# Kernel optimization log

Measured on AMD Instinct MI355X. Metric: run time of the kernel, lower is better.

## Reference

```python
import jax, jax.numpy as jnp
import numpy as np
from jax import lax


def setup_inputs() -> dict:
    key = jax.random.key(0)
    k1, k2, k3 = jax.random.split(key, 3)
    B, T, dimIn, dimH = 64, 2048, 128, 256
    x = jax.random.normal(k1, (B, T, dimIn), dtype=jnp.float32)
    h = jnp.zeros((B, dimH), dtype=jnp.float32)
    # torch nn.Linear(dimIn+dimH, dimH): weight [dimH, dimIn+dimH], bias [dimH]
    fan_in = dimIn + dimH
    bound = 1.0 / np.sqrt(fan_in)
    W = jax.random.uniform(k2, (dimH, fan_in), minval=-bound, maxval=bound, dtype=jnp.float32)
    b = jax.random.uniform(k3, (dimH,), minval=-bound, maxval=bound, dtype=jnp.float32)
    return {"x": x, "h": h, "W": W, "b": b}


def reference(x, h, W, b):
    # x: [B, T, dimIn], h: [B, H], W: [H, dimIn+H], b: [H]
    dimIn = x.shape[-1]
    Wx = W[:, :dimIn]   # [H, dimIn] -- acts on x part of concat
    Wh = W[:, dimIn:]   # [H, H]     -- acts on h part of concat
    # Precompute the input projection for all timesteps in one GEMM.
    xw = jnp.einsum('btd,hd->bth', x, Wx) + b  # [B, T, H]

    def step(h_prev, xw_t):
        h_new = jnp.tanh(xw_t + h_prev @ Wh.T)  # tanh(Linear(cat(x,h)))
        return h_new, h_new

    _, res = lax.scan(step, h, jnp.swapaxes(xw, 0, 1))  # res: [T, B, H]
    return jnp.swapaxes(res, 0, 1)  # [B, T, H]
```

## Files before the change

kernel.cpp:

```cpp
#include <hip/hip_runtime.h>
#include <hip/hip_fp16.h>

#define TSEQ  2048
#define BATCH 64
#define DIN   128
#define DH    256
#define WSTR  384
#define NCH   (TSEQ / 16)

typedef __fp16 h2    __attribute__((ext_vector_type(2)));
typedef __fp16 f16x8 __attribute__((ext_vector_type(8)));
typedef float  f32x4 __attribute__((ext_vector_type(4)));

static __device__ __forceinline__ h2 bc_h2(unsigned int u) {
    return __builtin_bit_cast(h2, u);
}

#define DPP_XOR1(v) __builtin_bit_cast(float, \
    __builtin_amdgcn_mov_dpp(__builtin_bit_cast(int, (v)), 0xB1, 0xF, 0xF, true))
#define DPP_XOR2(v) __builtin_bit_cast(float, \
    __builtin_amdgcn_mov_dpp(__builtin_bit_cast(int, (v)), 0x4E, 0xF, 0xF, true))

__global__ __launch_bounds__(256) void xw_gemm(const float* __restrict__ x,
                                               const float* __restrict__ W,
                                               const float* __restrict__ bias,
                                               float* __restrict__ out) {
    __shared__ __align__(16) __fp16 af[64][136];

    const int tid  = threadIdx.x;
    const int lane = tid & 63;
    const int wv   = tid >> 6;
    const int row0 = blockIdx.x * 64;
    const int nlo  = lane & 15;
    const int quad = lane >> 4;

    {
        const int r  = tid >> 2;
        const int c0 = (tid & 3) * 32;
        const float4* xr = (const float4*)(x + (size_t)(row0 + r) * DIN) + (tid & 3) * 8;
#pragma unroll
        for (int i = 0; i < 4; ++i) {
            float4 f0 = xr[2 * i];
            float4 f1 = xr[2 * i + 1];
            f16x8 v;
            v[0]=(__fp16)f0.x; v[1]=(__fp16)f0.y; v[2]=(__fp16)f0.z; v[3]=(__fp16)f0.w;
            v[4]=(__fp16)f1.x; v[5]=(__fp16)f1.y; v[6]=(__fp16)f1.z; v[7]=(__fp16)f1.w;
            *(f16x8*)&af[r][c0 + i * 8] = v;
        }
    }

    f16x8 bfr[4][4];
#pragma unroll
    for (int n0 = 0; n0 < 4; ++n0) {
        const int n = wv * 64 + n0 * 16 + nlo;
        const float* wr = W + (size_t)n * WSTR;
#pragma unroll
        for (int kk = 0; kk < 4; ++kk) {
            const int k = kk * 32 + quad * 8;
            float4 f0 = *(const float4*)(wr + k);
            float4 f1 = *(const float4*)(wr + k + 4);
            f16x8 v;
            v[0]=(__fp16)f0.x; v[1]=(__fp16)f0.y; v[2]=(__fp16)f0.z; v[3]=(__fp16)f0.w;
            v[4]=(__fp16)f1.x; v[5]=(__fp16)f1.y; v[6]=(__fp16)f1.z; v[7]=(__fp16)f1.w;
            bfr[n0][kk] = v;
        }
    }
    __syncthreads();

    f32x4 acc[4][4];
#pragma unroll
    for (int m0 = 0; m0 < 4; ++m0)
#pragma unroll
        for (int n0 = 0; n0 < 4; ++n0) acc[m0][n0] = (f32x4)0.0f;

#pragma unroll
    for (int kk = 0; kk < 4; ++kk) {
#pragma unroll
        for (int m0 = 0; m0 < 4; ++m0) {
            f16x8 a = *(const f16x8*)&af[m0 * 16 + nlo][kk * 32 + quad * 8];
#pragma unroll
            for (int n0 = 0; n0 < 4; ++n0)
                acc[m0][n0] = __builtin_amdgcn_mfma_f32_16x16x32_f16(
                                  a, bfr[n0][kk], acc[m0][n0], 0, 0, 0);
        }
    }

#pragma unroll
    for (int n0 = 0; n0 < 4; ++n0) {
        const int col = wv * 64 + n0 * 16 + nlo;
        const float bn = bias[col];
#pragma unroll
        for (int m0 = 0; m0 < 4; ++m0)
#pragma unroll
            for (int r = 0; r < 4; ++r) {
                const int row = row0 + m0 * 16 + quad * 4 + r;
                out[(size_t)row * DH + col] = acc[m0][n0][r] + bn;
            }
    }
}

__global__ __launch_bounds__(256, 1) void rnn_scan(const float* __restrict__ W,
                                                   const float* __restrict__ h0,
                                                   float* __restrict__ out) {
    __shared__ __align__(16) __fp16 hseg[2][4][72];

    const int tid = threadIdx.x;
    const int b   = blockIdx.x;
    const int q   = tid & 3;
    const int g   = tid >> 2;
    const bool b0 = (q & 1) != 0;
    const bool b1 = (q >> 1) != 0;

    h2 w[4][32];
#pragma unroll
    for (int o = 0; o < 4; ++o) {
        const float* wr = W + (size_t)(4 * g + o) * WSTR + DIN + 64 * q;
#pragma unroll
        for (int i = 0; i < 16; ++i) {
            float4 f = *(const float4*)(wr + 4 * i);
            w[o][2 * i]     = h2{(__fp16)f.x, (__fp16)f.y};
            w[o][2 * i + 1] = h2{(__fp16)f.z, (__fp16)f.w};
        }
    }
#pragma unroll
    for (int o = 0; o < 4; ++o)
#pragma unroll
        for (int i = 0; i < 32; ++i)
            asm volatile("" : "+v"(w[o][i]));

    hseg[0][tid >> 6][tid & 63] = (__fp16)h0[(size_t)b * DH + tid];

    const float* gsrc = out + (size_t)b * TSEQ * DH + tid;
    float*       gdst = out + (size_t)b * TSEQ * DH + tid;

    float xwreg[16];
#pragma unroll
    for (int s = 0; s < 16; ++s) xwreg[s] = gsrc[(size_t)s * DH];

    asm volatile("s_waitcnt lgkmcnt(0)\n\ts_barrier" ::: "memory");

#pragma unroll 1
    for (int c = 0; c < NCH; ++c) {
        const float* gnext = gsrc + (size_t)(c + 1 < NCH ? c + 1 : 0) * (16 * DH);
        float*       gout  = gdst + (size_t)c * (16 * DH);

#pragma unroll
        for (int s = 0; s < 16; ++s) {
            const float xw_s = xwreg[s];
            xwreg[s] = gnext[(size_t)s * DH];
            const int p = s & 1;
            const uint4* hp = (const uint4*)&hseg[p][q][0];

            float P0 = 0.f, P1 = 0.f, P2 = 0.f, P3 = 0.f;
#pragma unroll
            for (int i = 0; i < 8; ++i) {
                uint4 v = hp[i];
                h2 ha = bc_h2(v.x), hb = bc_h2(v.y), hc = bc_h2(v.z), hd = bc_h2(v.w);
                P0 = __builtin_amdgcn_fdot2(w[0][4*i], ha, P0, false);
                P1 = __builtin_amdgcn_fdot2(w[1][4*i], ha, P1, false);
                P2 = __builtin_amdgcn_fdot2(w[2][4*i], ha, P2, false);
                P3 = __builtin_amdgcn_fdot2(w[3][4*i], ha, P3, false);
                P0 = __builtin_amdgcn_fdot2(w[0][4*i+1], hb, P0, false);
                P1 = __builtin_amdgcn_fdot2(w[1][4*i+1], hb, P1, false);
                P2 = __builtin_amdgcn_fdot2(w[2][4*i+1], hb, P2, false);
                P3 = __builtin_amdgcn_fdot2(w[3][4*i+1], hb, P3, false);
                P0 = __builtin_amdgcn_fdot2(w[0][4*i+2], hc, P0, false);
                P1 = __builtin_amdgcn_fdot2(w[1][4*i+2], hc, P1, false);
                P2 = __builtin_amdgcn_fdot2(w[2][4*i+2], hc, P2, false);
                P3 = __builtin_amdgcn_fdot2(w[3][4*i+2], hc, P3, false);
                P0 = __builtin_amdgcn_fdot2(w[0][4*i+3], hd, P0, false);
                P1 = __builtin_amdgcn_fdot2(w[1][4*i+3], hd, P1, false);
                P2 = __builtin_amdgcn_fdot2(w[2][4*i+3], hd, P2, false);
                P3 = __builtin_amdgcn_fdot2(w[3][4*i+3], hd, P3, false);
            }

            float sendA = b0 ? P0 : P1;
            float sendB = b0 ? P2 : P3;
            float keepA = b0 ? P1 : P0;
            float keepB = b0 ? P3 : P2;
            float S0 = keepA + DPP_XOR1(sendA);
            float S1 = keepB + DPP_XOR1(sendB);
            float send2 = b1 ? S0 : S1;
            float keep2 = b1 ? S1 : S0;
            float dot = keep2 + DPP_XOR2(send2);

            float pre = xw_s + dot;
            float e  = __expf(2.0f * pre);
            float hn = 1.0f - 2.0f * __builtin_amdgcn_rcpf(e + 1.0f);

            hseg[p ^ 1][tid >> 6][tid & 63] = (__fp16)hn;
            gout[(size_t)s * DH] = hn;

            asm volatile("s_waitcnt lgkmcnt(0)\n\ts_barrier" ::: "memory");
        }
    }
}

extern "C" void kernel_launch(void* const* d_in, const int* in_sizes, int n_in,
                              void* d_out, int out_size, void* d_ws, size_t ws_size,
                              hipStream_t stream) {
    const float* x    = (const float*)d_in[0];
    const float* h0   = (const float*)d_in[1];
    const float* W    = (const float*)d_in[2];
    const float* bias = (const float*)d_in[3];
    float* out = (float*)d_out;

    xw_gemm<<<BATCH * TSEQ / 64, 256, 0, stream>>>(x, W, bias, out);
    rnn_scan<<<BATCH, 256, 0, stream>>>(W, h0, out);
}
```

Baseline: 1.239 ms.

## Split recurrent dot product over eight lanes with XOR-permuted weight rows

Result: faster. 994.7 us (-19.7%).

```diff
diff --git a/kernel.cpp b/kernel.cpp
--- a/kernel.cpp
+++ b/kernel.cpp
@@ -20,6 +20,8 @@
     __builtin_amdgcn_mov_dpp(__builtin_bit_cast(int, (v)), 0xB1, 0xF, 0xF, true))
 #define DPP_XOR2(v) __builtin_bit_cast(float, \
     __builtin_amdgcn_mov_dpp(__builtin_bit_cast(int, (v)), 0x4E, 0xF, 0xF, true))
+#define DPP_XOR8(v) __builtin_bit_cast(float, \
+    __builtin_amdgcn_mov_dpp(__builtin_bit_cast(int, (v)), 0x128, 0xF, 0xF, true))
 
 __global__ __launch_bounds__(256) void xw_gemm(const float* __restrict__ x,
                                                const float* __restrict__ W,
@@ -102,33 +104,31 @@
 __global__ __launch_bounds__(256, 1) void rnn_scan(const float* __restrict__ W,
                                                    const float* __restrict__ h0,
                                                    float* __restrict__ out) {
-    __shared__ __align__(16) __fp16 hseg[2][4][72];
+    __shared__ __align__(16) __fp16 hseg[2][8][40];
 
     const int tid = threadIdx.x;
     const int b   = blockIdx.x;
-    const int q   = tid & 3;
-    const int g   = tid >> 2;
-    const bool b0 = (q & 1) != 0;
-    const bool b1 = (q >> 1) != 0;
-
-    h2 w[4][32];
-#pragma unroll
-    for (int o = 0; o < 4; ++o) {
-        const float* wr = W + (size_t)(4 * g + o) * WSTR + DIN + 64 * q;
-#pragma unroll
-        for (int i = 0; i < 16; ++i) {
-            float4 f = *(const float4*)(wr + 4 * i);
-            w[o][2 * i]     = h2{(__fp16)f.x, (__fp16)f.y};
-            w[o][2 * i + 1] = h2{(__fp16)f.z, (__fp16)f.w};
-        }
-    }
-#pragma unroll
-    for (int o = 0; o < 4; ++o)
-#pragma unroll
-        for (int i = 0; i < 32; ++i)
-            asm volatile("" : "+v"(w[o][i]));
-
-    hseg[0][tid >> 6][tid & 63] = (__fp16)h0[(size_t)b * DH + tid];
+    const int sig = (tid & 3) | ((tid & 8) >> 1);
+
+    h2 w[8][16];
+#pragma unroll
+    for (int r = 0; r < 8; ++r) {
+        const int rho = (r & 3) | ((r & 4) << 1);
+        const float* wr = W + (size_t)(tid ^ rho) * WSTR + DIN + 32 * sig;
+#pragma unroll
+        for (int j = 0; j < 8; ++j) {
+            float4 f = *(const float4*)(wr + 4 * j);
+            w[r][2 * j]     = h2{(__fp16)f.x, (__fp16)f.y};
+            w[r][2 * j + 1] = h2{(__fp16)f.z, (__fp16)f.w};
+        }
+    }
+#pragma unroll
+    for (int r = 0; r < 8; ++r)
+#pragma unroll
+        for (int i = 0; i < 16; ++i)
+            asm volatile("" : "+v"(w[r][i]));
+
+    hseg[0][tid >> 5][tid & 31] = (__fp16)h0[(size_t)b * DH + tid];
 
     const float* gsrc = out + (size_t)b * TSEQ * DH + tid;
     float*       gdst = out + (size_t)b * TSEQ * DH + tid;
@@ -149,46 +149,37 @@
             const float xw_s = xwreg[s];
             xwreg[s] = gnext[(size_t)s * DH];
             const int p = s & 1;
-            const uint4* hp = (const uint4*)&hseg[p][q][0];
-
-            float P0 = 0.f, P1 = 0.f, P2 = 0.f, P3 = 0.f;
-#pragma unroll
-            for (int i = 0; i < 8; ++i) {
-                uint4 v = hp[i];
+            const uint4* hp = (const uint4*)&hseg[p][sig][0];
+
+            float P[8];
+#pragma unroll
+            for (int r = 0; r < 8; ++r) P[r] = 0.f;
+#pragma unroll
+            for (int i4 = 0; i4 < 4; ++i4) {
+                uint4 v = hp[i4];
                 h2 ha = bc_h2(v.x), hb = bc_h2(v.y), hc = bc_h2(v.z), hd = bc_h2(v.w);
-                P0 = __builtin_amdgcn_fdot2(w[0][4*i], ha, P0, false);
-                P1 = __builtin_amdgcn_fdot2(w[1][4*i], ha, P1, false);
-                P2 = __builtin_amdgcn_fdot2(w[2][4*i], ha, P2, false);
-                P3 = __builtin_amdgcn_fdot2(w[3][4*i], ha, P3, false);
-                P0 = __builtin_amdgcn_fdot2(w[0][4*i+1], hb, P0, false);
-                P1 = __builtin_amdgcn_fdot2(w[1][4*i+1], hb, P1, false);
-                P2 = __builtin_amdgcn_fdot2(w[2][4*i+1], hb, P2, false);
-                P3 = __builtin_amdgcn_fdot2(w[3][4*i+1], hb, P3, false);
-                P0 = __builtin_amdgcn_fdot2(w[0][4*i+2], hc, P0, false);
-                P1 = __builtin_amdgcn_fdot2(w[1][4*i+2], hc, P1, false);
-                P2 = __builtin_amdgcn_fdot2(w[2][4*i+2], hc, P2, false);
-                P3 = __builtin_amdgcn_fdot2(w[3][4*i+2], hc, P3, false);
-                P0 = __builtin_amdgcn_fdot2(w[0][4*i+3], hd, P0, false);
-                P1 = __builtin_amdgcn_fdot2(w[1][4*i+3], hd, P1, false);
-                P2 = __builtin_amdgcn_fdot2(w[2][4*i+3], hd, P2, false);
-                P3 = __builtin_amdgcn_fdot2(w[3][4*i+3], hd, P3, false);
+#pragma unroll
+                for (int r = 0; r < 8; ++r) {
+                    P[r] = __builtin_amdgcn_fdot2(w[r][4*i4+0], ha, P[r], false);
+                    P[r] = __builtin_amdgcn_fdot2(w[r][4*i4+1], hb, P[r], false);
+                    P[r] = __builtin_amdgcn_fdot2(w[r][4*i4+2], hc, P[r], false);
+                    P[r] = __builtin_amdgcn_fdot2(w[r][4*i4+3], hd, P[r], false);
+                }
             }
 
-            float sendA = b0 ? P0 : P1;
-            float sendB = b0 ? P2 : P3;
-            float keepA = b0 ? P1 : P0;
-            float keepB = b0 ? P3 : P2;
-            float S0 = keepA + DPP_XOR1(sendA);
-            float S1 = keepB + DPP_XOR1(sendB);
-            float send2 = b1 ? S0 : S1;
-            float keep2 = b1 ? S1 : S0;
-            float dot = keep2 + DPP_XOR2(send2);
+            float S0 = P[0] + DPP_XOR1(P[1]);
+            float S1 = P[2] + DPP_XOR1(P[3]);
+            float S2 = P[4] + DPP_XOR1(P[5]);
+            float S3 = P[6] + DPP_XOR1(P[7]);
+            float T0 = S0 + DPP_XOR2(S1);
+            float T1 = S2 + DPP_XOR2(S3);
+            float dot = T0 + DPP_XOR8(T1);
 
             float pre = xw_s + dot;
             float e  = __expf(2.0f * pre);
             float hn = 1.0f - 2.0f * __builtin_amdgcn_rcpf(e + 1.0f);
 
-            hseg[p ^ 1][tid >> 6][tid & 63] = (__fp16)hn;
+            hseg[p ^ 1][tid >> 5][tid & 31] = (__fp16)hn;
             gout[(size_t)s * DH] = hn;
 
             asm volatile("s_waitcnt lgkmcnt(0)\n\ts_barrier" ::: "memory");
```
